# Kernel tuning notes

Hardware: AMD Instinct MI355X
Metric: run time of the kernel (lower is better)

The kernel has to match this reference:

```python
import jax, jax.numpy as jnp
import numpy as np

B, T, D, H, E, K = 8, 1024, 1024, 16, 8, 2
HS = D // H  # head size
LN_EPS = 1e-5


def setup_inputs() -> dict:
    key = jax.random.key(0)
    ks = jax.random.split(key, 12)
    s = 0.02
    return {
        "x":  jax.random.normal(ks[0], (B, T, D), jnp.float32),
        "Wq": jax.random.normal(ks[1], (H, D, HS), jnp.float32) * s,
        "Wk": jax.random.normal(ks[2], (H, D, HS), jnp.float32) * s,
        "Wv": jax.random.normal(ks[3], (H, D, HS), jnp.float32) * s,
        "Wg": jax.random.normal(ks[4], (D, E), jnp.float32) * s,
        "W1": jax.random.normal(ks[5], (E, D, 4 * D), jnp.float32) * s,
        "b1": jnp.zeros((E, 4 * D), jnp.float32),
        "W2": jax.random.normal(ks[6], (E, 4 * D, D), jnp.float32) * s,
        "b2": jnp.zeros((E, D), jnp.float32),
        "g1": jnp.ones((D,), jnp.float32),
        "be1": jnp.zeros((D,), jnp.float32),
        "g2": jnp.ones((D,), jnp.float32),
        "be2": jnp.zeros((D,), jnp.float32),
    }


def _layernorm(h, g, b):
    mu = jnp.mean(h, axis=-1, keepdims=True)
    var = jnp.mean(jnp.square(h - mu), axis=-1, keepdims=True)
    return (h - mu) * jax.lax.rsqrt(var + LN_EPS) * g + b


def _attention(x, Wq, Wk, Wv):
    # per-head projections (no bias)
    q = jnp.einsum('btd,hde->bhte', x, Wq)
    k = jnp.einsum('btd,hde->bhte', x, Wk)
    v = jnp.einsum('btd,hde->bhte', x, Wv)
    # NOTE: original scales by C**-0.5 where C = x.shape[-1] = n_embed
    scores = jnp.einsum('bhte,bhse->bhts', q, k) * (D ** -0.5)
    causal = jnp.tril(jnp.ones((T, T), bool))
    scores = jnp.where(causal, scores, -jnp.inf)
    attn = jax.nn.softmax(scores, axis=-1)  # dropout = identity (eval)
    out = jnp.einsum('bhts,bhse->bhte', attn, v)
    # concat heads: [B,H,T,HS] -> [B,T,H*HS]
    return out.transpose(0, 2, 1, 3).reshape(B, T, D)


def _moe(x, Wg, W1, b1, W2, b2):
    xs = x.reshape(-1, D)                       # [N, D]
    logits = xs @ Wg                            # [N, E]
    w, sel = jax.lax.top_k(logits, K)           # [N, K]
    w = jax.nn.softmax(w.astype(jnp.float32), axis=-1).astype(x.dtype)
    # combine per-token per-expert weight: [N, E]
    we = jnp.sum(w[..., None] * (sel[..., None] == jnp.arange(E)), axis=1)
    res = jnp.zeros_like(xs)
    for e in range(E):  # fixed small expert count
        h = jax.nn.relu(xs @ W1[e] + b1[e])     # [N, 4D]
        y = h @ W2[e] + b2[e]                   # [N, D]
        res = res + we[:, e:e + 1] * y
    return res.reshape(x.shape)


def reference(x, Wq, Wk, Wv, Wg, W1, b1, W2, b2, g1, be1, g2, be2):
    out = x + _layernorm(_attention(x, Wq, Wk, Wv), g1, be1)
    out = out + _layernorm(_moe(x, Wg, W1, b1, W2, b2), g2, be2)
    return out
```

## Files before the change

### kernel.cpp

```cpp
#include <hip/hip_runtime.h>

#define B_    8
#define T_    1024
#define D_    1024
#define H_    16
#define HS_   64
#define E_    8
#define DFF   4096
#define NTOK  8192
#define NROW  16384

typedef unsigned short u16;
typedef unsigned int   u32;
typedef __attribute__((ext_vector_type(8))) short bf8;
typedef __attribute__((ext_vector_type(4))) float f4;

__device__ __forceinline__ u16 f2bf(float f) {
  u32 u = __float_as_uint(f);
  u32 r = (u + 0x7FFFu + ((u >> 16) & 1u)) >> 16;
  return (u16)r;
}
__device__ __forceinline__ float bf2f(u16 h) {
  return __uint_as_float(((u32)h) << 16);
}

__device__ __forceinline__ f4 mfma16(bf8 a, bf8 b, f4 c) {
  return __builtin_amdgcn_mfma_f32_16x16x32_bf16(a, b, c, 0, 0, 0);
}

typedef const __attribute__((address_space(1))) void* gas_ptr;
typedef __attribute__((address_space(3))) void* las_ptr;
__device__ __forceinline__ void async16(const void* g, void* l) {
  __builtin_amdgcn_global_load_lds((gas_ptr)g, (las_ptr)l, 16, 0, 0);
}

__global__ __launch_bounds__(256) void cvt_x_kernel(const float* __restrict__ x,
                                                    u16* __restrict__ xbf) {
  int i = blockIdx.x * 256 + threadIdx.x;
  float4 v = ((const float4*)x)[i];
  ushort4 o;
  o.x = f2bf(v.x); o.y = f2bf(v.y); o.z = f2bf(v.z); o.w = f2bf(v.w);
  ((ushort4*)xbf)[i] = o;
}

__global__ __launch_bounds__(256) void transpose_cvt_kernel(
    const float* __restrict__ src, u16* __restrict__ dst,
    int R, int C, size_t sStride, size_t dStride) {
  __shared__ float t[32][33];
  src += (size_t)blockIdx.z * sStride;
  dst += (size_t)blockIdx.z * dStride;
  int r0 = blockIdx.x * 32, c0 = blockIdx.y * 32;
  int tx = threadIdx.x & 31, ty = threadIdx.x >> 5;
#pragma unroll
  for (int i = 0; i < 32; i += 8)
    t[ty + i][tx] = src[(size_t)(r0 + ty + i) * C + (c0 + tx)];
  __syncthreads();
#pragma unroll
  for (int i = 0; i < 32; i += 8)
    dst[(size_t)(c0 + ty + i) * R + (r0 + tx)] = f2bf(t[tx][ty + i]);
}

__global__ __launch_bounds__(256) void vtrans_kernel(const u16* __restrict__ qkv,
                                                     u16* __restrict__ Vt) {
  __shared__ u16 t[32][33];
  int bh = blockIdx.z, b = bh >> 4, h = bh & 15;
  const u16* Vg = qkv + (size_t)(32 + h) * NTOK * HS_ + (size_t)b * T_ * HS_;
  u16* Vp = Vt + (size_t)bh * HS_ * T_;
  int t0 = blockIdx.x * 32, c0 = blockIdx.y * 32;
  int tx = threadIdx.x & 31, ty = threadIdx.x >> 5;
#pragma unroll
  for (int i = 0; i < 32; i += 8)
    t[ty + i][tx] = Vg[(size_t)(t0 + ty + i) * HS_ + c0 + tx];
  __syncthreads();
#pragma unroll
  for (int i = 0; i < 32; i += 8)
    Vp[(size_t)(c0 + ty + i) * T_ + t0 + tx] = t[tx][ty + i];
}

__global__ __launch_bounds__(256) void gating_kernel(
    const float* __restrict__ x, const float* __restrict__ Wg,
    int* __restrict__ sel, float* __restrict__ wgt) {
  int wave = threadIdx.x >> 6, lane = threadIdx.x & 63;
  int t = blockIdx.x * 4 + wave;
  int e = lane & 7, grp = lane >> 3;
  const float* xr = x + (size_t)t * D_;
  float acc = 0.f;
  for (int i = 0; i < 128; ++i) {
    int d = grp + i * 8;
    acc += xr[d] * Wg[d * 8 + e];
  }
  acc += __shfl_xor(acc, 8);
  acc += __shfl_xor(acc, 16);
  acc += __shfl_xor(acc, 32);
  float lg[8];
#pragma unroll
  for (int j = 0; j < 8; ++j) lg[j] = __shfl(acc, j);
  int s0 = 0; float v0 = lg[0];
#pragma unroll
  for (int j = 1; j < 8; ++j) if (lg[j] > v0) { v0 = lg[j]; s0 = j; }
  int s1 = -1; float v1 = -3.4e38f;
#pragma unroll
  for (int j = 0; j < 8; ++j) if (j != s0 && lg[j] > v1) { v1 = lg[j]; s1 = j; }
  if (lane == 0) {
    float dd = __expf(v1 - v0);
    float w0 = 1.f / (1.f + dd);
    sel[2 * t]     = s0; sel[2 * t + 1] = s1;
    wgt[2 * t]     = w0; wgt[2 * t + 1] = dd * w0;
  }
}

__global__ __launch_bounds__(256) void offsets_kernel(const int* __restrict__ sel,
                                                      int* __restrict__ meta) {
  __shared__ int hist[E_];
  int tid = threadIdx.x;
  if (tid < E_) hist[tid] = 0;
  __syncthreads();
  for (int i = tid; i < NROW; i += 256) atomicAdd(&hist[sel[i]], 1);
  __syncthreads();
  if (tid == 0) {
    int s = 0, mb = 0;
    for (int e = 0; e < E_; ++e) {
      int c = hist[e];
      meta[e] = c; meta[8 + e] = s; meta[16 + e] = mb;
      s += c; mb += (c + 127) >> 7;
    }
    meta[24] = mb;
  }
}

__global__ __launch_bounds__(256) void assign_kernel(
    const int* __restrict__ sel, const float* __restrict__ wgt,
    const int* __restrict__ meta, int* __restrict__ gidx,
    float* __restrict__ gw, int* __restrict__ rowmap) {
  int e = blockIdx.x, tid = threadIdx.x, lane = tid & 63, wv = tid >> 6;
  __shared__ int wsum[4];
  __shared__ int carry;
  if (tid == 0) carry = meta[8 + e];
  __syncthreads();
  for (int base = 0; base < NROW; base += 256) {
    int idx = base + tid;
    int f = (sel[idx] == e) ? 1 : 0;
    unsigned long long mask = __ballot(f);
    int pre = __popcll(mask & ((1ull << lane) - 1ull));
    if (lane == 0) wsum[wv] = __popcll(mask);
    __syncthreads();
    int woff = 0;
    for (int w = 0; w < wv; ++w) woff += wsum[w];
    int cb = carry;
    if (f) {
      int pos = cb + woff + pre;
      gidx[pos] = idx >> 1;
      gw[pos] = wgt[idx];
      rowmap[idx] = pos;
    }
    __syncthreads();
    if (tid == 0) carry = cb + wsum[0] + wsum[1] + wsum[2] + wsum[3];
    __syncthreads();
  }
}

template <int MODE>
__global__ __launch_bounds__(256) void gemm_bt(
    const u16* __restrict__ A, const u16* __restrict__ Bt,
    u16* __restrict__ outB, const float* __restrict__ bias,
    const int* __restrict__ meta, const int* __restrict__ gidx, int K) {
  int n0 = blockIdx.y * 128;
  int n_e = 0, off = 0, m0, e = 0;
  const u16* Ap = A;
  const u16* Bp = Bt;
  if constexpr (MODE != 0) {
    int xb = blockIdx.x;
#pragma unroll
    for (int j = 1; j < 8; ++j) if (meta[16 + j] <= xb) e = j;
    n_e = meta[e];
    off = meta[8 + e];
    m0 = (xb - meta[16 + e]) * 128;
    if (m0 >= n_e) return;
    if constexpr (MODE == 1) {
      Bp = Bt + (size_t)e * DFF * 1024;
    } else {
      Ap = A + (size_t)off * DFF;
      Bp = Bt + (size_t)e * 1024 * DFF;
    }
  } else {
    m0 = blockIdx.x * 128;
  }

  __shared__ __align__(16) u16 As[128 * 64];
  __shared__ __align__(16) u16 Bs[128 * 64];
  int tid = threadIdx.x, lane = tid & 63, wave = tid >> 6;
  int wm = wave >> 1, wn = wave & 1, ml = lane & 15, quad = lane >> 4;
  int lrow = lane >> 3;
  int gcol = ((lane & 7) ^ lrow) * 8;

  const u16* arow[4];
  const u16* brow[4];
#pragma unroll
  for (int r = 0; r < 4; ++r) {
    int row = wave * 32 + r * 8;
    int ra = m0 + row + lrow;
    if constexpr (MODE == 1) {
      int rr = ra < n_e ? ra : n_e - 1;
      arow[r] = Ap + (size_t)gidx[off + rr] * 1024 + gcol;
    } else if constexpr (MODE == 2) {
      int rr = ra < n_e ? ra : n_e - 1;
      arow[r] = Ap + (size_t)rr * DFF + gcol;
    } else {
      arow[r] = Ap + (size_t)ra * 1024 + gcol;
    }
    brow[r] = Bp + (size_t)(n0 + row + lrow) * K + gcol;
  }

  f4 acc[4][4];
#pragma unroll
  for (int i = 0; i < 4; ++i)
#pragma unroll
    for (int j = 0; j < 4; ++j) acc[i][j] = (f4){0.f, 0.f, 0.f, 0.f};

  int mlx = ml & 7;
  for (int k0 = 0; k0 < K; k0 += 64) {
    __syncthreads();
#pragma unroll
    for (int r = 0; r < 4; ++r) {
      int row = wave * 32 + r * 8;
      async16(arow[r] + k0, &As[row * 64]);
      async16(brow[r] + k0, &Bs[row * 64]);
    }
    __syncthreads();
#pragma unroll
    for (int kk = 0; kk < 64; kk += 32) {
      int p = (((kk >> 3) + quad) ^ mlx) * 8;
      bf8 af[4], bfr[4];
#pragma unroll
      for (int mi = 0; mi < 4; ++mi)
        af[mi] = *(const bf8*)&As[(wm * 64 + mi * 16 + ml) * 64 + p];
#pragma unroll
      for (int ni = 0; ni < 4; ++ni)
        bfr[ni] = *(const bf8*)&Bs[(wn * 64 + ni * 16 + ml) * 64 + p];
#pragma unroll
      for (int mi = 0; mi < 4; ++mi)
#pragma unroll
        for (int ni = 0; ni < 4; ++ni)
          acc[mi][ni] = mfma16(af[mi], bfr[ni], acc[mi][ni]);
    }
  }

#pragma unroll
  for (int mi = 0; mi < 4; ++mi)
#pragma unroll
    for (int ni = 0; ni < 4; ++ni)
#pragma unroll
      for (int rg = 0; rg < 4; ++rg) {
        int m = m0 + wm * 64 + mi * 16 + quad * 4 + rg;
        int n = n0 + wn * 64 + ni * 16 + ml;
        float v = acc[mi][ni][rg];
        if constexpr (MODE == 0) {
          int pl = n >> 6, col = n & 63;
          outB[(size_t)pl * NTOK * HS_ + (size_t)m * HS_ + col] = f2bf(v);
        } else if constexpr (MODE == 1) {
          if (m < n_e) {
            float hv = v + bias[e * DFF + n];
            outB[(size_t)(off + m) * DFF + n] = f2bf(fmaxf(hv, 0.f));
          }
        } else {
          if (m < n_e) {
            outB[(size_t)(off + m) * 1024 + n] = f2bf(v + bias[e * 1024 + n]);
          }
        }
      }
}

__global__ __launch_bounds__(256) void attn_kernel(const u16* __restrict__ qkv,
                                                   const u16* __restrict__ Vt,
                                                   float* __restrict__ attn_out) {
  int qt = blockIdx.x, bh = blockIdx.y;
  int b = bh >> 4, h = bh & 15;
  int q0 = qt * 64;
  const u16* Qg = qkv + (size_t)h * NTOK * HS_ + (size_t)b * T_ * HS_;
  const u16* Kg = qkv + (size_t)(16 + h) * NTOK * HS_ + (size_t)b * T_ * HS_;
  const u16* Vp = Vt + (size_t)bh * HS_ * T_;
  __shared__ __align__(16) u16 Qs[64 * 72];
  __shared__ __align__(16) u16 Ks[64 * 72];
  __shared__ __align__(16) u16 Vs[64 * 72];
  __shared__ __align__(16) u16 Ps[64 * 72];
  int tid = threadIdx.x, lane = tid & 63, wave = tid >> 6;
  int ml = lane & 15, quad = lane >> 4;

  for (int i = tid; i < 512; i += 256) {
    int r = i >> 3, c = (i & 7) * 8;
    *(uint4*)&Qs[r * 72 + c] = *(const uint4*)(Qg + (size_t)(q0 + r) * HS_ + c);
  }

  f4 acc_o[4];
  float m_[4], l_[4];
#pragma unroll
  for (int i = 0; i < 4; ++i) {
    acc_o[i] = (f4){0.f, 0.f, 0.f, 0.f};
    m_[i] = -1e30f; l_[i] = 0.f;
  }

  for (int ck = 0; ck <= qt; ++ck) {
    int kv0 = ck * 64;
    __syncthreads();
    for (int i = tid; i < 512; i += 256) {
      int r = i >> 3, c = (i & 7) * 8;
      *(uint4*)&Ks[r * 72 + c] = *(const uint4*)(Kg + (size_t)(kv0 + r) * HS_ + c);
      *(uint4*)&Vs[r * 72 + c] = *(const uint4*)(Vp + (size_t)r * T_ + kv0 + c);
    }
    __syncthreads();

    f4 sacc[4];
#pragma unroll
    for (int nt = 0; nt < 4; ++nt) sacc[nt] = (f4){0.f, 0.f, 0.f, 0.f};
#pragma unroll
    for (int kk = 0; kk < 64; kk += 32) {
      bf8 a = *(const bf8*)&Qs[(wave * 16 + ml) * 72 + kk + quad * 8];
#pragma unroll
      for (int nt = 0; nt < 4; ++nt) {
        bf8 bk = *(const bf8*)&Ks[(nt * 16 + ml) * 72 + kk + quad * 8];
        sacc[nt] = mfma16(a, bk, sacc[nt]);
      }
    }

    bool dm = (kv0 == q0);
    float pv[4][4], mx[4];
#pragma unroll
    for (int rg = 0; rg < 4; ++rg) {
      int gq = q0 + wave * 16 + quad * 4 + rg;
      float mm = -1e30f;
#pragma unroll
      for (int nt = 0; nt < 4; ++nt) {
        float s = sacc[nt][rg] * 0.03125f;
        if (dm && (kv0 + nt * 16 + ml) > gq) s = -1e30f;
        pv[nt][rg] = s;
        mm = fmaxf(mm, s);
      }
      mx[rg] = mm;
    }
#pragma unroll
    for (int off = 1; off < 16; off <<= 1)
#pragma unroll
      for (int rg = 0; rg < 4; ++rg) mx[rg] = fmaxf(mx[rg], __shfl_xor(mx[rg], off));

    float al[4], rs[4];
#pragma unroll
    for (int rg = 0; rg < 4; ++rg) {
      float mn = fmaxf(m_[rg], mx[rg]);
      al[rg] = __expf(m_[rg] - mn);
      m_[rg] = mn;
      float r = 0.f;
#pragma unroll
      for (int nt = 0; nt < 4; ++nt) {
        float ev = __expf(pv[nt][rg] - mn);
        pv[nt][rg] = ev;
        r += ev;
      }
      rs[rg] = r;
    }
#pragma unroll
    for (int off = 1; off < 16; off <<= 1)
#pragma unroll
      for (int rg = 0; rg < 4; ++rg) rs[rg] += __shfl_xor(rs[rg], off);

#pragma unroll
    for (int rg = 0; rg < 4; ++rg) {
      l_[rg] = al[rg] * l_[rg] + rs[rg];
#pragma unroll
      for (int nt = 0; nt < 4; ++nt) {
        acc_o[nt][rg] *= al[rg];
        Ps[(wave * 16 + quad * 4 + rg) * 72 + nt * 16 + ml] = f2bf(pv[nt][rg]);
      }
    }

#pragma unroll
    for (int kk = 0; kk < 64; kk += 32) {
      bf8 a = *(const bf8*)&Ps[(wave * 16 + ml) * 72 + kk + quad * 8];
#pragma unroll
      for (int ci = 0; ci < 4; ++ci) {
        bf8 bv = *(const bf8*)&Vs[(ci * 16 + ml) * 72 + kk + quad * 8];
        acc_o[ci] = mfma16(a, bv, acc_o[ci]);
      }
    }
  }

#pragma unroll
  for (int rg = 0; rg < 4; ++rg) {
    float inv = 1.f / l_[rg];
    int gq = q0 + wave * 16 + quad * 4 + rg;
    float* orow = attn_out + (size_t)(b * T_ + gq) * D_ + h * HS_;
#pragma unroll
    for (int ci = 0; ci < 4; ++ci) orow[ci * 16 + ml] = acc_o[ci][rg] * inv;
  }
}

__global__ __launch_bounds__(256) void final_kernel(
    const float* __restrict__ x, const float* __restrict__ attn,
    const u16* __restrict__ Y, const int* __restrict__ rowmap,
    const float* __restrict__ wgt,
    const float* __restrict__ g1, const float* __restrict__ be1,
    const float* __restrict__ g2, const float* __restrict__ be2,
    float* __restrict__ out) {
  int t = blockIdx.x, tid = threadIdx.x;
  int lane = tid & 63, wave = tid >> 6;
  float4 av = ((const float4*)(attn + (size_t)t * D_))[tid];
  int r0 = rowmap[2 * t], r1 = rowmap[2 * t + 1];
  float w0 = wgt[2 * t], w1 = wgt[2 * t + 1];
  ushort4 y0 = ((const ushort4*)(Y + (size_t)r0 * D_))[tid];
  ushort4 y1 = ((const ushort4*)(Y + (size_t)r1 * D_))[tid];
  float4 mv;
  mv.x = w0 * bf2f(y0.x) + w1 * bf2f(y1.x);
  mv.y = w0 * bf2f(y0.y) + w1 * bf2f(y1.y);
  mv.z = w0 * bf2f(y0.z) + w1 * bf2f(y1.z);
  mv.w = w0 * bf2f(y0.w) + w1 * bf2f(y1.w);

  float sa = av.x + av.y + av.z + av.w;
  float qa = av.x * av.x + av.y * av.y + av.z * av.z + av.w * av.w;
  float sm = mv.x + mv.y + mv.z + mv.w;
  float qm = mv.x * mv.x + mv.y * mv.y + mv.z * mv.z + mv.w * mv.w;
#pragma unroll
  for (int off = 1; off < 64; off <<= 1) {
    sa += __shfl_xor(sa, off);
    qa += __shfl_xor(qa, off);
    sm += __shfl_xor(sm, off);
    qm += __shfl_xor(qm, off);
  }
  __shared__ float red[4][4];
  if (lane == 0) { red[wave][0] = sa; red[wave][1] = qa; red[wave][2] = sm; red[wave][3] = qm; }
  __syncthreads();
  sa = red[0][0] + red[1][0] + red[2][0] + red[3][0];
  qa = red[0][1] + red[1][1] + red[2][1] + red[3][1];
  sm = red[0][2] + red[1][2] + red[2][2] + red[3][2];
  qm = red[0][3] + red[1][3] + red[2][3] + red[3][3];
  const float inv_d = 1.f / 1024.f;
  float mu1 = sa * inv_d, var1 = qa * inv_d - mu1 * mu1;
  float mu2 = sm * inv_d, var2 = qm * inv_d - mu2 * mu2;
  float rs1 = rsqrtf(var1 + 1e-5f), rs2 = rsqrtf(var2 + 1e-5f);

  float4 xv = ((const float4*)(x + (size_t)t * D_))[tid];
  float4 g1v = ((const float4*)g1)[tid], b1v = ((const float4*)be1)[tid];
  float4 g2v = ((const float4*)g2)[tid], b2v = ((const float4*)be2)[tid];
  float4 o;
  o.x = xv.x + (av.x - mu1) * rs1 * g1v.x + b1v.x + (mv.x - mu2) * rs2 * g2v.x + b2v.x;
  o.y = xv.y + (av.y - mu1) * rs1 * g1v.y + b1v.y + (mv.y - mu2) * rs2 * g2v.y + b2v.y;
  o.z = xv.z + (av.z - mu1) * rs1 * g1v.z + b1v.z + (mv.z - mu2) * rs2 * g2v.z + b2v.z;
  o.w = xv.w + (av.w - mu1) * rs1 * g1v.w + b1v.w + (mv.w - mu2) * rs2 * g2v.w + b2v.w;
  ((float4*)(out + (size_t)t * D_))[tid] = o;
}

extern "C" void kernel_launch(void* const* d_in, const int* in_sizes, int n_in,
                              void* d_out, int out_size, void* d_ws, size_t ws_size,
                              hipStream_t stream) {
  const float* x   = (const float*)d_in[0];
  const float* Wq  = (const float*)d_in[1];
  const float* Wk  = (const float*)d_in[2];
  const float* Wv  = (const float*)d_in[3];
  const float* Wg  = (const float*)d_in[4];
  const float* W1  = (const float*)d_in[5];
  const float* b1  = (const float*)d_in[6];
  const float* W2  = (const float*)d_in[7];
  const float* b2  = (const float*)d_in[8];
  const float* g1  = (const float*)d_in[9];
  const float* be1 = (const float*)d_in[10];
  const float* g2  = (const float*)d_in[11];
  const float* be2 = (const float*)d_in[12];
  float* out = (float*)d_out;

  char* ws = (char*)d_ws;
  size_t off = 0;
  auto alloc = [&](size_t bytes) -> void* {
    void* p = ws + off;
    off = (off + bytes + 255) & ~(size_t)255;
    return p;
  };
  u16*   xbf    = (u16*)alloc((size_t)NTOK * D_ * 2);
  u16*   wqkvt  = (u16*)alloc((size_t)48 * 64 * 1024 * 2);
  u16*   w1t    = (u16*)alloc((size_t)E_ * DFF * 1024 * 2);
  u16*   w2t    = (u16*)alloc((size_t)E_ * 1024 * DFF * 2);
  u16*   qkv    = (u16*)alloc((size_t)48 * NTOK * HS_ * 2);
  float* attn   = (float*)alloc((size_t)NTOK * D_ * 4);
  u16*   Hbuf   = (u16*)alloc((size_t)NROW * DFF * 2);
  u16*   Ybuf   = (u16*)alloc((size_t)NROW * 1024 * 2);
  int*   meta   = (int*)alloc(256);
  int*   sel    = (int*)alloc(NROW * 4);
  float* wgt    = (float*)alloc(NROW * 4);
  int*   gidx   = (int*)alloc(NROW * 4);
  float* gw     = (float*)alloc(NROW * 4);
  int*   rowmap = (int*)alloc(NROW * 4);
  u16*   Vt     = Hbuf;
  (void)ws_size; (void)in_sizes; (void)n_in; (void)out_size; (void)gw;

  cvt_x_kernel<<<NTOK * D_ / 1024, 256, 0, stream>>>(x, xbf);
  transpose_cvt_kernel<<<dim3(32, 2, 16), 256, 0, stream>>>(Wq, wqkvt, 1024, 64, 65536, 65536);
  transpose_cvt_kernel<<<dim3(32, 2, 16), 256, 0, stream>>>(Wk, wqkvt + 16 * 65536, 1024, 64, 65536, 65536);
  transpose_cvt_kernel<<<dim3(32, 2, 16), 256, 0, stream>>>(Wv, wqkvt + 32 * 65536, 1024, 64, 65536, 65536);
  transpose_cvt_kernel<<<dim3(32, 128, 8), 256, 0, stream>>>(W1, w1t, 1024, 4096, (size_t)1024 * 4096, (size_t)1024 * 4096);
  transpose_cvt_kernel<<<dim3(128, 32, 8), 256, 0, stream>>>(W2, w2t, 4096, 1024, (size_t)4096 * 1024, (size_t)4096 * 1024);

  gating_kernel<<<NTOK / 4, 256, 0, stream>>>(x, Wg, sel, wgt);
  offsets_kernel<<<1, 256, 0, stream>>>(sel, meta);
  assign_kernel<<<E_, 256, 0, stream>>>(sel, wgt, meta, gidx, gw, rowmap);

  gemm_bt<0><<<dim3(64, 24), 256, 0, stream>>>(xbf, wqkvt, qkv, nullptr, nullptr, nullptr, 1024);
  vtrans_kernel<<<dim3(32, 2, 128), 256, 0, stream>>>(qkv, Vt);
  attn_kernel<<<dim3(16, 128), 256, 0, stream>>>(qkv, Vt, attn);

  gemm_bt<1><<<dim3(136, 32), 256, 0, stream>>>(xbf, w1t, Hbuf, b1, meta, gidx, 1024);
  gemm_bt<2><<<dim3(136, 8), 256, 0, stream>>>(Hbuf, w2t, Ybuf, b2, meta, gidx, 4096);

  final_kernel<<<NTOK, 256, 0, stream>>>(x, attn, Ybuf, rowmap, wgt, g1, be1, g2, be2, out);
}
```

Baseline: 1.117 ms.

## Double-buffer GEMM LDS tiles and switch to 32x32x16 MFMA

The shared GEMM kernel (QKV projection and both expert MLP GEMMs) now keeps two LDS buffers per operand, so the async global-to-LDS load for the next K slice is issued before the current slice is consumed. This removes one barrier per iteration and overlaps loading with MFMA work. Each wave computes its 64x64 tile with four 32x32x16 bf16 MFMAs per K step instead of sixteen 16x16x32 ones, which cuts LDS fragment reads, and the epilogue is remapped to the 32x32 output layout with the bias loaded once per column. The cost is twice the LDS (64KB per block), which may lower occupancy.

```diff
diff --git a/kernel.cpp b/kernel.cpp
--- a/kernel.cpp
+++ b/kernel.cpp
@@ -14,6 +14,7 @@
 typedef unsigned int   u32;
 typedef __attribute__((ext_vector_type(8))) short bf8;
 typedef __attribute__((ext_vector_type(4))) float f4;
+typedef __attribute__((ext_vector_type(16))) float f16f;
 
 __device__ __forceinline__ u16 f2bf(float f) {
   u32 u = __float_as_uint(f);
@@ -26,6 +27,9 @@
 
 __device__ __forceinline__ f4 mfma16(bf8 a, bf8 b, f4 c) {
   return __builtin_amdgcn_mfma_f32_16x16x32_bf16(a, b, c, 0, 0, 0);
+}
+__device__ __forceinline__ f16f mfma32(bf8 a, bf8 b, f16f c) {
+  return __builtin_amdgcn_mfma_f32_32x32x16_bf16(a, b, c, 0, 0, 0);
 }
 
 typedef const __attribute__((address_space(1))) void* gas_ptr;
@@ -186,10 +190,11 @@
     m0 = blockIdx.x * 128;
   }
 
-  __shared__ __align__(16) u16 As[128 * 64];
-  __shared__ __align__(16) u16 Bs[128 * 64];
+  __shared__ __align__(16) u16 As[2][128 * 64];
+  __shared__ __align__(16) u16 Bs[2][128 * 64];
   int tid = threadIdx.x, lane = tid & 63, wave = tid >> 6;
-  int wm = wave >> 1, wn = wave & 1, ml = lane & 15, quad = lane >> 4;
+  int wm = wave >> 1, wn = wave & 1;
+  int l31 = lane & 31, lhi = lane >> 5;
   int lrow = lane >> 3;
   int gcol = ((lane & 7) ^ lrow) * 8;
 
@@ -211,63 +216,70 @@
     brow[r] = Bp + (size_t)(n0 + row + lrow) * K + gcol;
   }
 
-  f4 acc[4][4];
-#pragma unroll
-  for (int i = 0; i < 4; ++i)
-#pragma unroll
-    for (int j = 0; j < 4; ++j) acc[i][j] = (f4){0.f, 0.f, 0.f, 0.f};
-
-  int mlx = ml & 7;
-  for (int k0 = 0; k0 < K; k0 += 64) {
-    __syncthreads();
+  f16f acc[2][2];
+#pragma unroll
+  for (int i = 0; i < 2; ++i)
+#pragma unroll
+    for (int j = 0; j < 2; ++j) acc[i][j] = (f16f)0.f;
+
+  auto stage = [&](int k0, int bsel) {
 #pragma unroll
     for (int r = 0; r < 4; ++r) {
       int row = wave * 32 + r * 8;
-      async16(arow[r] + k0, &As[row * 64]);
-      async16(brow[r] + k0, &Bs[row * 64]);
-    }
+      async16(arow[r] + k0, &As[bsel][row * 64]);
+      async16(brow[r] + k0, &Bs[bsel][row * 64]);
+    }
+  };
+
+  int nit = K >> 6;
+  stage(0, 0);
+  for (int it = 0; it < nit; ++it) {
     __syncthreads();
-#pragma unroll
-    for (int kk = 0; kk < 64; kk += 32) {
-      int p = (((kk >> 3) + quad) ^ mlx) * 8;
-      bf8 af[4], bfr[4];
-#pragma unroll
-      for (int mi = 0; mi < 4; ++mi)
-        af[mi] = *(const bf8*)&As[(wm * 64 + mi * 16 + ml) * 64 + p];
-#pragma unroll
-      for (int ni = 0; ni < 4; ++ni)
-        bfr[ni] = *(const bf8*)&Bs[(wn * 64 + ni * 16 + ml) * 64 + p];
-#pragma unroll
-      for (int mi = 0; mi < 4; ++mi)
-#pragma unroll
-        for (int ni = 0; ni < 4; ++ni)
-          acc[mi][ni] = mfma16(af[mi], bfr[ni], acc[mi][ni]);
-    }
-  }
-
-#pragma unroll
-  for (int mi = 0; mi < 4; ++mi)
-#pragma unroll
-    for (int ni = 0; ni < 4; ++ni)
-#pragma unroll
-      for (int rg = 0; rg < 4; ++rg) {
-        int m = m0 + wm * 64 + mi * 16 + quad * 4 + rg;
-        int n = n0 + wn * 64 + ni * 16 + ml;
-        float v = acc[mi][ni][rg];
+    if (it + 1 < nit) stage((it + 1) << 6, (it + 1) & 1);
+    const u16* Ab = As[it & 1];
+    const u16* Bb = Bs[it & 1];
+#pragma unroll
+    for (int ks = 0; ks < 4; ++ks) {
+      int p = (((ks << 1) + lhi) ^ (lane & 7)) * 8;
+      bf8 af[2], bfr[2];
+#pragma unroll
+      for (int mi = 0; mi < 2; ++mi)
+        af[mi] = *(const bf8*)&Ab[(wm * 64 + mi * 32 + l31) * 64 + p];
+#pragma unroll
+      for (int ni = 0; ni < 2; ++ni)
+        bfr[ni] = *(const bf8*)&Bb[(wn * 64 + ni * 32 + l31) * 64 + p];
+#pragma unroll
+      for (int mi = 0; mi < 2; ++mi)
+#pragma unroll
+        for (int ni = 0; ni < 2; ++ni)
+          acc[mi][ni] = mfma32(af[mi], bfr[ni], acc[mi][ni]);
+    }
+  }
+
+#pragma unroll
+  for (int mi = 0; mi < 2; ++mi)
+#pragma unroll
+    for (int ni = 0; ni < 2; ++ni) {
+      int n = n0 + wn * 64 + ni * 32 + l31;
+      float bv = 0.f;
+      if constexpr (MODE == 1) bv = bias[e * DFF + n];
+      if constexpr (MODE == 2) bv = bias[e * 1024 + n];
+#pragma unroll
+      for (int r = 0; r < 16; ++r) {
+        int m = m0 + wm * 64 + mi * 32 + (r & 3) + 8 * (r >> 2) + 4 * lhi;
+        float v = acc[mi][ni][r];
         if constexpr (MODE == 0) {
           int pl = n >> 6, col = n & 63;
           outB[(size_t)pl * NTOK * HS_ + (size_t)m * HS_ + col] = f2bf(v);
         } else if constexpr (MODE == 1) {
-          if (m < n_e) {
-            float hv = v + bias[e * DFF + n];
-            outB[(size_t)(off + m) * DFF + n] = f2bf(fmaxf(hv, 0.f));
-          }
+          if (m < n_e)
+            outB[(size_t)(off + m) * DFF + n] = f2bf(fmaxf(v + bv, 0.f));
         } else {
-          if (m < n_e) {
-            outB[(size_t)(off + m) * 1024 + n] = f2bf(v + bias[e * 1024 + n]);
-          }
+          if (m < n_e)
+            outB[(size_t)(off + m) * 1024 + n] = f2bf(v + bv);
         }
       }
+    }
 }
 
 __global__ __launch_bounds__(256) void attn_kernel(const u16* __restrict__ qkv,
```

New measurement: 1.238 ms. 1.11x slower.
